# Performance work log

Measured on AMD Instinct MI355X. Metric: run time of the kernel, lower is better.

## Reference

```python
import jax, jax.numpy as jnp
import numpy as np

B, S, E = 4, 2048, 1024
N, H = 16, 64  # n_head, per-head hidden


def setup_inputs() -> dict:
    key = jax.random.key(0)
    k1, k2, k3, k4, k5 = jax.random.split(key, 5)
    scale_in = 1.0 / np.sqrt(E)
    scale_h = 1.0 / np.sqrt(N * H)
    return {
        "x": jax.random.normal(k1, (B, S, E), dtype=jnp.float32),
        "W_qkv": jax.random.uniform(k2, (E, 3 * N * H), minval=-scale_in, maxval=scale_in, dtype=jnp.float32),
        "b_qkv": jax.random.uniform(k3, (3 * N * H,), minval=-scale_in, maxval=scale_in, dtype=jnp.float32),
        "W_out": jax.random.uniform(k4, (N * H, E), minval=-scale_h, maxval=scale_h, dtype=jnp.float32),
        "b_out": jax.random.uniform(k5, (E,), minval=-scale_h, maxval=scale_h, dtype=jnp.float32),
    }


def reference(x, W_qkv, b_qkv, W_out, b_out):
    b, s, e = x.shape
    qkv = x @ W_qkv + b_qkv                      # [B,S,3NH]
    q, k, v = jnp.split(qkv, 3, axis=-1)
    q = q.reshape(b, s, N, H).transpose(0, 2, 1, 3)  # [B,N,S,H]
    k = k.reshape(b, s, N, H).transpose(0, 2, 1, 3)
    v = v.reshape(b, s, N, H).transpose(0, 2, 1, 3)
    inv_scale = jnp.asarray(1.0 / np.sqrt(H), dtype=x.dtype)
    attn = jnp.einsum('bnqh,bnkh->bnqk', q, k) * inv_scale  # [B,N,S,S]
    causal = jnp.tril(jnp.ones((s, s), dtype=bool))
    attn = jnp.where(causal[None, None], attn, jnp.asarray(-jnp.inf, dtype=attn.dtype))
    attn = jax.nn.softmax(attn, axis=-1)
    out = jnp.einsum('bnqk,bnkh->bnqh', attn, v)  # [B,N,S,H]
    out = out.transpose(0, 2, 1, 3).reshape(b, s, N * H)
    return out @ W_out + b_out
```

## Files before the change

kernel.cpp:

```cpp
#include <hip/hip_runtime.h>
#include <hip/hip_bf16.h>

typedef __attribute__((ext_vector_type(8))) short s16x8;
typedef __attribute__((ext_vector_type(4))) short s16x4;
typedef __attribute__((ext_vector_type(4))) float f32x4;

#define MFMA16(a, b, c) __builtin_amdgcn_mfma_f32_16x16x32_bf16(a, b, c, 0, 0, 0)

__device__ __forceinline__ short f2bf(float f) {
  unsigned int x = __builtin_bit_cast(unsigned int, f);
  x += 0x7fffu + ((x >> 16) & 1u);
  return (short)(x >> 16);
}

__device__ __forceinline__ int cperm(int k) {
  return ((k & 12) << 1) | ((k >> 4) << 2) | (k & 3);
}

#define LDT 40

__global__ void cvt_f32_bf16(const float* __restrict__ in, short* __restrict__ out, int n) {
  int idx = blockIdx.x * blockDim.x + threadIdx.x;
  int stride = gridDim.x * blockDim.x;
  for (int i = idx * 4; i < n; i += stride * 4) {
    float4 v = *(const float4*)(in + i);
    s16x4 o;
    o[0] = f2bf(v.x); o[1] = f2bf(v.y); o[2] = f2bf(v.z); o[3] = f2bf(v.w);
    *(s16x4*)(out + i) = o;
  }
}

__global__ __launch_bounds__(256) void gemm_qkv(
    const short* __restrict__ X, const short* __restrict__ W,
    const float* __restrict__ bias,
    short* __restrict__ Qo, short* __restrict__ Ko, short* __restrict__ Vo) {
  const int N = 3072, Kd = 1024;
  __shared__ short As[128 * LDT];
  __shared__ short Bs[128 * LDT];
  int t = threadIdx.x;
  int nTN = N / 128;
  int m0 = (blockIdx.x / nTN) * 128;
  int n0 = (blockIdx.x % nTN) * 128;
  int lane = t & 63, w = t >> 6;
  int wr = (w >> 1) * 64, wc = (w & 1) * 64;
  int r = lane & 15, g = lane >> 4;

  int ar = t >> 1;
  int ak = (t & 1) << 4;
  int bk = t & 31;
  int bc = (t >> 5) << 4;
  int cbk = cperm(bk);

  f32x4 acc[4][4];
  const f32x4 z4 = {0.f, 0.f, 0.f, 0.f};
#pragma unroll
  for (int i = 0; i < 4; ++i)
#pragma unroll
    for (int j = 0; j < 4; ++j) acc[i][j] = z4;

  for (int kt = 0; kt < Kd; kt += 32) {
    if (kt) __syncthreads();
    const short* xr = X + (size_t)(m0 + ar) * Kd + kt + ak;
    s16x8 va0 = *(const s16x8*)(xr);
    s16x8 va1 = *(const s16x8*)(xr + 8);
    short* Ad = &As[ar * LDT];
    *(s16x4*)(Ad + cperm(ak))      = __builtin_shufflevector(va0, va0, 0, 1, 2, 3);
    *(s16x4*)(Ad + cperm(ak + 4))  = __builtin_shufflevector(va0, va0, 4, 5, 6, 7);
    *(s16x4*)(Ad + cperm(ak + 8))  = __builtin_shufflevector(va1, va1, 0, 1, 2, 3);
    *(s16x4*)(Ad + cperm(ak + 12)) = __builtin_shufflevector(va1, va1, 4, 5, 6, 7);
    const short* wrp = W + (size_t)(kt + bk) * N + n0 + bc;
    s16x8 vb0 = *(const s16x8*)(wrp);
    s16x8 vb1 = *(const s16x8*)(wrp + 8);
#pragma unroll
    for (int i = 0; i < 8; ++i) Bs[(bc + i) * LDT + cbk] = vb0[i];
#pragma unroll
    for (int i = 0; i < 8; ++i) Bs[(bc + 8 + i) * LDT + cbk] = vb1[i];
    __syncthreads();

    s16x8 af[4], bfr[4];
#pragma unroll
    for (int mi = 0; mi < 4; ++mi)
      af[mi] = *(const s16x8*)(&As[(wr + mi * 16 + r) * LDT + g * 8]);
#pragma unroll
    for (int ni = 0; ni < 4; ++ni)
      bfr[ni] = *(const s16x8*)(&Bs[(wc + ni * 16 + r) * LDT + g * 8]);
#pragma unroll
    for (int mi = 0; mi < 4; ++mi)
#pragma unroll
      for (int ni = 0; ni < 4; ++ni)
        acc[mi][ni] = MFMA16(af[mi], bfr[ni], acc[mi][ni]);
  }

#pragma unroll
  for (int ni = 0; ni < 4; ++ni) {
    int col = n0 + wc + ni * 16 + r;
    float bv = bias[col];
    int which = col >> 10;
    int rem = col & 1023;
    int head = rem >> 6, h = rem & 63;
    short* dst = (which == 0) ? Qo : (which == 1) ? Ko : Vo;
#pragma unroll
    for (int mi = 0; mi < 4; ++mi)
#pragma unroll
      for (int e = 0; e < 4; ++e) {
        int row = m0 + wr + mi * 16 + g * 4 + e;
        int b = row >> 11, s = row & 2047;
        dst[((size_t)(b * 16 + head) * 2048 + s) * 64 + h] = f2bf(acc[mi][ni][e] + bv);
      }
  }
}

__global__ __launch_bounds__(256) void gemm_out(
    const short* __restrict__ X, const short* __restrict__ W,
    const float* __restrict__ bias, float* __restrict__ Out) {
  const int N = 1024, Kd = 1024;
  __shared__ short As[128 * LDT];
  __shared__ short Bs[128 * LDT];
  int t = threadIdx.x;
  int nTN = N / 128;
  int m0 = (blockIdx.x / nTN) * 128;
  int n0 = (blockIdx.x % nTN) * 128;
  int lane = t & 63, w = t >> 6;
  int wr = (w >> 1) * 64, wc = (w & 1) * 64;
  int r = lane & 15, g = lane >> 4;
  int ar = t >> 1, ak = (t & 1) << 4;
  int bk = t & 31, bc = (t >> 5) << 4;
  int cbk = cperm(bk);

  f32x4 acc[4][4];
  const f32x4 z4 = {0.f, 0.f, 0.f, 0.f};
#pragma unroll
  for (int i = 0; i < 4; ++i)
#pragma unroll
    for (int j = 0; j < 4; ++j) acc[i][j] = z4;

  for (int kt = 0; kt < Kd; kt += 32) {
    if (kt) __syncthreads();
    const short* xr = X + (size_t)(m0 + ar) * Kd + kt + ak;
    s16x8 va0 = *(const s16x8*)(xr);
    s16x8 va1 = *(const s16x8*)(xr + 8);
    short* Ad = &As[ar * LDT];
    *(s16x4*)(Ad + cperm(ak))      = __builtin_shufflevector(va0, va0, 0, 1, 2, 3);
    *(s16x4*)(Ad + cperm(ak + 4))  = __builtin_shufflevector(va0, va0, 4, 5, 6, 7);
    *(s16x4*)(Ad + cperm(ak + 8))  = __builtin_shufflevector(va1, va1, 0, 1, 2, 3);
    *(s16x4*)(Ad + cperm(ak + 12)) = __builtin_shufflevector(va1, va1, 4, 5, 6, 7);
    const short* wrp = W + (size_t)(kt + bk) * N + n0 + bc;
    s16x8 vb0 = *(const s16x8*)(wrp);
    s16x8 vb1 = *(const s16x8*)(wrp + 8);
#pragma unroll
    for (int i = 0; i < 8; ++i) Bs[(bc + i) * LDT + cbk] = vb0[i];
#pragma unroll
    for (int i = 0; i < 8; ++i) Bs[(bc + 8 + i) * LDT + cbk] = vb1[i];
    __syncthreads();

    s16x8 af[4], bfr[4];
#pragma unroll
    for (int mi = 0; mi < 4; ++mi)
      af[mi] = *(const s16x8*)(&As[(wr + mi * 16 + r) * LDT + g * 8]);
#pragma unroll
    for (int ni = 0; ni < 4; ++ni)
      bfr[ni] = *(const s16x8*)(&Bs[(wc + ni * 16 + r) * LDT + g * 8]);
#pragma unroll
    for (int mi = 0; mi < 4; ++mi)
#pragma unroll
      for (int ni = 0; ni < 4; ++ni)
        acc[mi][ni] = MFMA16(af[mi], bfr[ni], acc[mi][ni]);
  }

#pragma unroll
  for (int ni = 0; ni < 4; ++ni) {
    int col = n0 + wc + ni * 16 + r;
    float bv = bias[col];
#pragma unroll
    for (int mi = 0; mi < 4; ++mi)
#pragma unroll
      for (int e = 0; e < 4; ++e) {
        int row = m0 + wr + mi * 16 + g * 4 + e;
        Out[(size_t)row * N + col] = acc[mi][ni][e] + bv;
      }
  }
}

#define LDTV 72
__global__ __launch_bounds__(256) void attn(
    const short* __restrict__ Qb, const short* __restrict__ Kb,
    const short* __restrict__ Vb, short* __restrict__ Ob) {
  const int S = 2048, H = 64;
  int bid = blockIdx.x;
  int qt = 15 - (bid >> 6);
  int bn = bid & 63;
  int batch = bn >> 4, head = bn & 15;
  int q0 = qt * 128;
  int t = threadIdx.x, lane = t & 63, w = t >> 6;
  int r = lane & 15, g = lane >> 4;
  int qw = q0 + w * 32;

  const short* Qh = Qb + (size_t)bn * S * H;
  const short* Kh = Kb + (size_t)bn * S * H;
  const short* Vh = Vb + (size_t)bn * S * H;

  __shared__ short Vs[64 * LDTV];

  s16x8 qf[2][2];
#pragma unroll
  for (int n = 0; n < 2; ++n)
#pragma unroll
    for (int ks = 0; ks < 2; ++ks) {
      const short* qr = Qh + (size_t)(qw + n * 16 + r) * H + ks * 32 + g * 4;
      s16x4 lo = *(const s16x4*)(qr);
      s16x4 hi = *(const s16x4*)(qr + 16);
      qf[n][ks] = __builtin_shufflevector(lo, hi, 0, 1, 2, 3, 4, 5, 6, 7);
    }

  f32x4 o[2][4];
  const f32x4 z4 = {0.f, 0.f, 0.f, 0.f};
#pragma unroll
  for (int n = 0; n < 2; ++n)
#pragma unroll
    for (int hb = 0; hb < 4; ++hb) o[n][hb] = z4;
  float mrun[2] = {-__builtin_inff(), -__builtin_inff()};
  float lrun[2] = {0.f, 0.f};

  int ntiles = q0 / 64 + 2;

  int vr = lane;
  int hbase = w * 16;
  int vcol = ((vr >> 5) << 5) + cperm(vr & 31);

  s16x8 v0 = *(const s16x8*)(Vh + (size_t)vr * H + hbase);
  s16x8 v1 = *(const s16x8*)(Vh + (size_t)vr * H + hbase + 8);

  for (int tt = 0; tt < ntiles; ++tt) {
    int kv0 = tt * 64;
    if (tt) __syncthreads();
#pragma unroll
    for (int i = 0; i < 8; ++i) Vs[(hbase + i) * LDTV + vcol] = v0[i];
#pragma unroll
    for (int i = 0; i < 8; ++i) Vs[(hbase + 8 + i) * LDTV + vcol] = v1[i];
    __syncthreads();
    if (tt + 1 < ntiles) {
      const short* vp = Vh + (size_t)((tt + 1) * 64 + vr) * H + hbase;
      v0 = *(const s16x8*)(vp);
      v1 = *(const s16x8*)(vp + 8);
    }
    if (kv0 > qw + 31) continue;

    int mpmax = (qw + 31 - kv0) >> 4; if (mpmax > 3) mpmax = 3;
    bool need_mask = (kv0 + 63 > qw);

    s16x8 kf[4][2];
#pragma unroll
    for (int mp = 0; mp < 4; ++mp) {
      if (mp <= mpmax) {
#pragma unroll
        for (int ks = 0; ks < 2; ++ks) {
          const short* kr = Kh + (size_t)(kv0 + mp * 16 + r) * H + ks * 32 + g * 4;
          s16x4 lo = *(const s16x4*)(kr);
          s16x4 hi = *(const s16x4*)(kr + 16);
          kf[mp][ks] = __builtin_shufflevector(lo, hi, 0, 1, 2, 3, 4, 5, 6, 7);
        }
      }
    }

    float p[4][2][4];
    float rmax[2] = {-__builtin_inff(), -__builtin_inff()};
#pragma unroll
    for (int mp = 0; mp < 4; ++mp) {
      if (mp <= mpmax) {
        f32x4 st[2] = {z4, z4};
#pragma unroll
        for (int n = 0; n < 2; ++n)
#pragma unroll
          for (int ks = 0; ks < 2; ++ks)
            st[n] = MFMA16(kf[mp][ks], qf[n][ks], st[n]);
#pragma unroll
        for (int n = 0; n < 2; ++n)
#pragma unroll
          for (int e = 0; e < 4; ++e) {
            float v = st[n][e] * 0.125f;
            if (need_mask) {
              int kv = kv0 + mp * 16 + g * 4 + e;
              int q = qw + n * 16 + r;
              if (kv > q) v = -__builtin_inff();
            }
            p[mp][n][e] = v;
            rmax[n] = fmaxf(rmax[n], v);
          }
      } else {
#pragma unroll
        for (int n = 0; n < 2; ++n)
#pragma unroll
          for (int e = 0; e < 4; ++e) p[mp][n][e] = 0.f;
      }
    }

#pragma unroll
    for (int n = 0; n < 2; ++n) {
      rmax[n] = fmaxf(rmax[n], __shfl_xor(rmax[n], 16));
      rmax[n] = fmaxf(rmax[n], __shfl_xor(rmax[n], 32));
    }

#pragma unroll
    for (int n = 0; n < 2; ++n) {
      if (!__all(rmax[n] - mrun[n] <= 8.0f)) {
        float mnew = fmaxf(mrun[n], rmax[n]);
        float sc = __expf(mrun[n] - mnew);
        lrun[n] *= sc;
        mrun[n] = mnew;
#pragma unroll
        for (int e = 0; e < 4; ++e) {
          float bs = __shfl(sc, (lane & 48) + g * 4 + e);
#pragma unroll
          for (int hb = 0; hb < 4; ++hb) o[n][hb][e] *= bs;
        }
      }
    }

    float rsum[2] = {0.f, 0.f};
#pragma unroll
    for (int mp = 0; mp < 4; ++mp) {
      if (mp <= mpmax) {
#pragma unroll
        for (int n = 0; n < 2; ++n)
#pragma unroll
          for (int e = 0; e < 4; ++e) {
            float ev = __expf(p[mp][n][e] - mrun[n]);
            p[mp][n][e] = ev;
            rsum[n] += ev;
          }
      }
    }
#pragma unroll
    for (int n = 0; n < 2; ++n) {
      rsum[n] += __shfl_xor(rsum[n], 16);
      rsum[n] += __shfl_xor(rsum[n], 32);
      lrun[n] += rsum[n];
    }

    int kvhmax = mpmax >> 1;
#pragma unroll
    for (int kvh = 0; kvh < 2; ++kvh) {
      if (kvh > kvhmax) break;
      s16x8 pa[2];
#pragma unroll
      for (int n = 0; n < 2; ++n) {
        s16x8 tmp = {f2bf(p[2 * kvh][n][0]),     f2bf(p[2 * kvh][n][1]),
                     f2bf(p[2 * kvh][n][2]),     f2bf(p[2 * kvh][n][3]),
                     f2bf(p[2 * kvh + 1][n][0]), f2bf(p[2 * kvh + 1][n][1]),
                     f2bf(p[2 * kvh + 1][n][2]), f2bf(p[2 * kvh + 1][n][3])};
        pa[n] = tmp;
      }
#pragma unroll
      for (int hb = 0; hb < 4; ++hb) {
        s16x8 vf = *(const s16x8*)(&Vs[(hb * 16 + r) * LDTV + kvh * 32 + g * 8]);
#pragma unroll
        for (int n = 0; n < 2; ++n) o[n][hb] = MFMA16(pa[n], vf, o[n][hb]);
      }
    }
  }

#pragma unroll
  for (int n = 0; n < 2; ++n) {
    float il = 1.0f / lrun[n];
#pragma unroll
    for (int e = 0; e < 4; ++e) {
      float bv = __shfl(il, (lane & 48) + g * 4 + e);
      int s = qw + n * 16 + g * 4 + e;
#pragma unroll
      for (int hb = 0; hb < 4; ++hb) {
        int c = head * 64 + hb * 16 + r;
        Ob[(size_t)(batch * 2048 + s) * 1024 + c] = f2bf(o[n][hb][e] * bv);
      }
    }
  }
}

extern "C" void kernel_launch(void* const* d_in, const int* in_sizes, int n_in,
                              void* d_out, int out_size, void* d_ws, size_t ws_size,
                              hipStream_t stream) {
  const float* x    = (const float*)d_in[0];
  const float* Wqkv = (const float*)d_in[1];
  const float* bqkv = (const float*)d_in[2];
  const float* Wout = (const float*)d_in[3];
  const float* bout = (const float*)d_in[4];
  float* out = (float*)d_out;

  char* ws = (char*)d_ws;
  short* Xb    = (short*)(ws);
  short* Wqkvb = (short*)(ws + ((size_t)16 << 20));
  short* Woutb = (short*)(ws + ((size_t)22 << 20));
  short* Qb    = (short*)(ws + ((size_t)24 << 20));
  short* Kb    = (short*)(ws + ((size_t)40 << 20));
  short* Vb    = (short*)(ws + ((size_t)56 << 20));

  cvt_f32_bf16<<<2048, 256, 0, stream>>>(x, Xb, 4 * 2048 * 1024);
  cvt_f32_bf16<<<1024, 256, 0, stream>>>(Wqkv, 1024 * 3072 ? (short*)Wqkvb : Wqkvb, 1024 * 3072);
  cvt_f32_bf16<<<512, 256, 0, stream>>>(Wout, Woutb, 1024 * 1024);

  gemm_qkv<<<64 * 24, 256, 0, stream>>>(Xb, Wqkvb, bqkv, Qb, Kb, Vb);
  attn<<<64 * 16, 256, 0, stream>>>(Qb, Kb, Vb, Xb);
  gemm_out<<<64 * 8, 256, 0, stream>>>(Xb, Woutb, bout, out);
}
```

Before: 281.4 us.

## Pair causal query tiles per block, prefetch K fragments, fold scale into Q

Each attention block now handles two query tiles (qt and 15-qt), so every block does the same amount of causal work, and the grid is halved to 512 blocks. K fragments for the next tile are double-buffered in registers so their loads overlap the current tile's compute. The 1/sqrt(H) scale moves into the QKV GEMM epilogue, and the per-tile cross-lane row-sum reduction is deferred to the end. The cost is more register pressure from the two K buffers and fewer blocks in flight, which could lower occupancy.

```diff
diff --git a/kernel.cpp b/kernel.cpp
--- a/kernel.cpp
+++ b/kernel.cpp
@@ -99,13 +99,14 @@
     int rem = col & 1023;
     int head = rem >> 6, h = rem & 63;
     short* dst = (which == 0) ? Qo : (which == 1) ? Ko : Vo;
+    float qsc = (which == 0) ? 0.125f : 1.0f;
 #pragma unroll
     for (int mi = 0; mi < 4; ++mi)
 #pragma unroll
       for (int e = 0; e < 4; ++e) {
         int row = m0 + wr + mi * 16 + g * 4 + e;
         int b = row >> 11, s = row & 2047;
-        dst[((size_t)(b * 16 + head) * 2048 + s) * 64 + h] = f2bf(acc[mi][ni][e] + bv);
+        dst[((size_t)(b * 16 + head) * 2048 + s) * 64 + h] = f2bf((acc[mi][ni][e] + bv) * qsc);
       }
   }
 }
@@ -187,13 +188,11 @@
     const short* __restrict__ Vb, short* __restrict__ Ob) {
   const int S = 2048, H = 64;
   int bid = blockIdx.x;
-  int qt = 15 - (bid >> 6);
   int bn = bid & 63;
+  int pr = bid >> 6;
   int batch = bn >> 4, head = bn & 15;
-  int q0 = qt * 128;
   int t = threadIdx.x, lane = t & 63, w = t >> 6;
   int r = lane & 15, g = lane >> 4;
-  int qw = q0 + w * 32;
 
   const short* Qh = Qb + (size_t)bn * S * H;
   const short* Kh = Kb + (size_t)bn * S * H;
@@ -201,57 +200,40 @@
 
   __shared__ short Vs[64 * LDTV];
 
-  s16x8 qf[2][2];
-#pragma unroll
-  for (int n = 0; n < 2; ++n)
-#pragma unroll
-    for (int ks = 0; ks < 2; ++ks) {
-      const short* qr = Qh + (size_t)(qw + n * 16 + r) * H + ks * 32 + g * 4;
-      s16x4 lo = *(const s16x4*)(qr);
-      s16x4 hi = *(const s16x4*)(qr + 16);
-      qf[n][ks] = __builtin_shufflevector(lo, hi, 0, 1, 2, 3, 4, 5, 6, 7);
-    }
-
-  f32x4 o[2][4];
-  const f32x4 z4 = {0.f, 0.f, 0.f, 0.f};
-#pragma unroll
-  for (int n = 0; n < 2; ++n)
-#pragma unroll
-    for (int hb = 0; hb < 4; ++hb) o[n][hb] = z4;
-  float mrun[2] = {-__builtin_inff(), -__builtin_inff()};
-  float lrun[2] = {0.f, 0.f};
-
-  int ntiles = q0 / 64 + 2;
-
   int vr = lane;
   int hbase = w * 16;
   int vcol = ((vr >> 5) << 5) + cperm(vr & 31);
-
-  s16x8 v0 = *(const s16x8*)(Vh + (size_t)vr * H + hbase);
-  s16x8 v1 = *(const s16x8*)(Vh + (size_t)vr * H + hbase + 8);
-
-  for (int tt = 0; tt < ntiles; ++tt) {
-    int kv0 = tt * 64;
-    if (tt) __syncthreads();
-#pragma unroll
-    for (int i = 0; i < 8; ++i) Vs[(hbase + i) * LDTV + vcol] = v0[i];
-#pragma unroll
-    for (int i = 0; i < 8; ++i) Vs[(hbase + 8 + i) * LDTV + vcol] = v1[i];
-    __syncthreads();
-    if (tt + 1 < ntiles) {
-      const short* vp = Vh + (size_t)((tt + 1) * 64 + vr) * H + hbase;
-      v0 = *(const s16x8*)(vp);
-      v1 = *(const s16x8*)(vp + 8);
-    }
-    if (kv0 > qw + 31) continue;
-
-    int mpmax = (qw + 31 - kv0) >> 4; if (mpmax > 3) mpmax = 3;
-    bool need_mask = (kv0 + 63 > qw);
-
-    s16x8 kf[4][2];
-#pragma unroll
-    for (int mp = 0; mp < 4; ++mp) {
-      if (mp <= mpmax) {
+  const f32x4 z4 = {0.f, 0.f, 0.f, 0.f};
+
+#pragma unroll
+  for (int ph = 0; ph < 2; ++ph) {
+    int qt = ph ? pr : (15 - pr);
+    int q0 = qt * 128;
+    int qw = q0 + w * 32;
+    int ntiles = qt * 2 + 2;
+
+    s16x8 qf[2][2];
+#pragma unroll
+    for (int n = 0; n < 2; ++n)
+#pragma unroll
+      for (int ks = 0; ks < 2; ++ks) {
+        const short* qr = Qh + (size_t)(qw + n * 16 + r) * H + ks * 32 + g * 4;
+        s16x4 lo = *(const s16x4*)(qr);
+        s16x4 hi = *(const s16x4*)(qr + 16);
+        qf[n][ks] = __builtin_shufflevector(lo, hi, 0, 1, 2, 3, 4, 5, 6, 7);
+      }
+
+    f32x4 o[2][4];
+#pragma unroll
+    for (int n = 0; n < 2; ++n)
+#pragma unroll
+      for (int hb = 0; hb < 4; ++hb) o[n][hb] = z4;
+    float mrun[2] = {-__builtin_inff(), -__builtin_inff()};
+    float lsum[2] = {0.f, 0.f};
+
+    auto LOADK = [&](int kv0, s16x8 (&kf)[4][2]) {
+#pragma unroll
+      for (int mp = 0; mp < 4; ++mp)
 #pragma unroll
         for (int ks = 0; ks < 2; ++ks) {
           const short* kr = Kh + (size_t)(kv0 + mp * 16 + r) * H + ks * 32 + g * 4;
@@ -259,117 +241,143 @@
           s16x4 hi = *(const s16x4*)(kr + 16);
           kf[mp][ks] = __builtin_shufflevector(lo, hi, 0, 1, 2, 3, 4, 5, 6, 7);
         }
-      }
+    };
+
+    s16x8 v0 = *(const s16x8*)(Vh + (size_t)vr * H + hbase);
+    s16x8 v1 = *(const s16x8*)(Vh + (size_t)vr * H + hbase + 8);
+    s16x8 kfA[4][2], kfB[4][2];
+    LOADK(0, kfA);
+
+    auto TILE = [&](int tt, s16x8 (&kfc)[4][2], s16x8 (&kfn)[4][2]) {
+      int kv0 = tt * 64;
+      if (tt | ph) __syncthreads();
+#pragma unroll
+      for (int i = 0; i < 8; ++i) Vs[(hbase + i) * LDTV + vcol] = v0[i];
+#pragma unroll
+      for (int i = 0; i < 8; ++i) Vs[(hbase + 8 + i) * LDTV + vcol] = v1[i];
+      __syncthreads();
+      if (tt + 1 < ntiles) {
+        const short* vp = Vh + (size_t)((tt + 1) * 64 + vr) * H + hbase;
+        v0 = *(const s16x8*)(vp);
+        v1 = *(const s16x8*)(vp + 8);
+      }
+      int tn = tt + 1;
+      if (tn < ntiles && tn * 64 <= qw + 31) LOADK(tn * 64, kfn);
+      if (kv0 > qw + 31) return;
+
+      int mpmax = (qw + 31 - kv0) >> 4; if (mpmax > 3) mpmax = 3;
+      bool need_mask = (kv0 + 63 > qw);
+
+      float p[4][2][4];
+      float rmax[2] = {-__builtin_inff(), -__builtin_inff()};
+#pragma unroll
+      for (int mp = 0; mp < 4; ++mp) {
+        if (mp <= mpmax) {
+          f32x4 st[2] = {z4, z4};
+#pragma unroll
+          for (int n = 0; n < 2; ++n)
+#pragma unroll
+            for (int ks = 0; ks < 2; ++ks)
+              st[n] = MFMA16(kfc[mp][ks], qf[n][ks], st[n]);
+#pragma unroll
+          for (int n = 0; n < 2; ++n)
+#pragma unroll
+            for (int e = 0; e < 4; ++e) {
+              float v = st[n][e];
+              if (need_mask) {
+                int kv = kv0 + mp * 16 + g * 4 + e;
+                int q = qw + n * 16 + r;
+                if (kv > q) v = -__builtin_inff();
+              }
+              p[mp][n][e] = v;
+              rmax[n] = fmaxf(rmax[n], v);
+            }
+        } else {
+#pragma unroll
+          for (int n = 0; n < 2; ++n)
+#pragma unroll
+            for (int e = 0; e < 4; ++e) p[mp][n][e] = 0.f;
+        }
+      }
+
+#pragma unroll
+      for (int n = 0; n < 2; ++n) {
+        rmax[n] = fmaxf(rmax[n], __shfl_xor(rmax[n], 16));
+        rmax[n] = fmaxf(rmax[n], __shfl_xor(rmax[n], 32));
+      }
+
+#pragma unroll
+      for (int n = 0; n < 2; ++n) {
+        if (!__all(rmax[n] - mrun[n] <= 8.0f)) {
+          float mnew = fmaxf(mrun[n], rmax[n]);
+          float sc = __expf(mrun[n] - mnew);
+          lsum[n] *= sc;
+          mrun[n] = mnew;
+#pragma unroll
+          for (int e = 0; e < 4; ++e) {
+            float bs = __shfl(sc, (lane & 48) + g * 4 + e);
+#pragma unroll
+            for (int hb = 0; hb < 4; ++hb) o[n][hb][e] *= bs;
+          }
+        }
+      }
+
+#pragma unroll
+      for (int mp = 0; mp < 4; ++mp) {
+        if (mp <= mpmax) {
+#pragma unroll
+          for (int n = 0; n < 2; ++n)
+#pragma unroll
+            for (int e = 0; e < 4; ++e) {
+              float ev = __expf(p[mp][n][e] - mrun[n]);
+              p[mp][n][e] = ev;
+              lsum[n] += ev;
+            }
+        }
+      }
+
+      int kvhmax = mpmax >> 1;
+#pragma unroll
+      for (int kvh = 0; kvh < 2; ++kvh) {
+        if (kvh > kvhmax) break;
+        s16x8 pa[2];
+#pragma unroll
+        for (int n = 0; n < 2; ++n) {
+          s16x8 tmp = {f2bf(p[2 * kvh][n][0]),     f2bf(p[2 * kvh][n][1]),
+                       f2bf(p[2 * kvh][n][2]),     f2bf(p[2 * kvh][n][3]),
+                       f2bf(p[2 * kvh + 1][n][0]), f2bf(p[2 * kvh + 1][n][1]),
+                       f2bf(p[2 * kvh + 1][n][2]), f2bf(p[2 * kvh + 1][n][3])};
+          pa[n] = tmp;
+        }
+#pragma unroll
+        for (int hb = 0; hb < 4; ++hb) {
+          s16x8 vf = *(const s16x8*)(&Vs[(hb * 16 + r) * LDTV + kvh * 32 + g * 8]);
+#pragma unroll
+          for (int n = 0; n < 2; ++n) o[n][hb] = MFMA16(pa[n], vf, o[n][hb]);
+        }
+      }
+    };
+
+    for (int tt = 0; tt < ntiles; tt += 2) {
+      TILE(tt, kfA, kfB);
+      TILE(tt + 1, kfB, kfA);
     }
 
-    float p[4][2][4];
-    float rmax[2] = {-__builtin_inff(), -__builtin_inff()};
-#pragma unroll
-    for (int mp = 0; mp < 4; ++mp) {
-      if (mp <= mpmax) {
-        f32x4 st[2] = {z4, z4};
-#pragma unroll
-        for (int n = 0; n < 2; ++n)
-#pragma unroll
-          for (int ks = 0; ks < 2; ++ks)
-            st[n] = MFMA16(kf[mp][ks], qf[n][ks], st[n]);
-#pragma unroll
-        for (int n = 0; n < 2; ++n)
-#pragma unroll
-          for (int e = 0; e < 4; ++e) {
-            float v = st[n][e] * 0.125f;
-            if (need_mask) {
-              int kv = kv0 + mp * 16 + g * 4 + e;
-              int q = qw + n * 16 + r;
-              if (kv > q) v = -__builtin_inff();
-            }
-            p[mp][n][e] = v;
-            rmax[n] = fmaxf(rmax[n], v);
-          }
-      } else {
-#pragma unroll
-        for (int n = 0; n < 2; ++n)
-#pragma unroll
-          for (int e = 0; e < 4; ++e) p[mp][n][e] = 0.f;
-      }
-    }
-
 #pragma unroll
     for (int n = 0; n < 2; ++n) {
-      rmax[n] = fmaxf(rmax[n], __shfl_xor(rmax[n], 16));
-      rmax[n] = fmaxf(rmax[n], __shfl_xor(rmax[n], 32));
-    }
-
-#pragma unroll
-    for (int n = 0; n < 2; ++n) {
-      if (!__all(rmax[n] - mrun[n] <= 8.0f)) {
-        float mnew = fmaxf(mrun[n], rmax[n]);
-        float sc = __expf(mrun[n] - mnew);
-        lrun[n] *= sc;
-        mrun[n] = mnew;
-#pragma unroll
-        for (int e = 0; e < 4; ++e) {
-          float bs = __shfl(sc, (lane & 48) + g * 4 + e);
-#pragma unroll
-          for (int hb = 0; hb < 4; ++hb) o[n][hb][e] *= bs;
-        }
-      }
-    }
-
-    float rsum[2] = {0.f, 0.f};
-#pragma unroll
-    for (int mp = 0; mp < 4; ++mp) {
-      if (mp <= mpmax) {
-#pragma unroll
-        for (int n = 0; n < 2; ++n)
-#pragma unroll
-          for (int e = 0; e < 4; ++e) {
-            float ev = __expf(p[mp][n][e] - mrun[n]);
-            p[mp][n][e] = ev;
-            rsum[n] += ev;
-          }
-      }
-    }
-#pragma unroll
-    for (int n = 0; n < 2; ++n) {
-      rsum[n] += __shfl_xor(rsum[n], 16);
-      rsum[n] += __shfl_xor(rsum[n], 32);
-      lrun[n] += rsum[n];
-    }
-
-    int kvhmax = mpmax >> 1;
-#pragma unroll
-    for (int kvh = 0; kvh < 2; ++kvh) {
-      if (kvh > kvhmax) break;
-      s16x8 pa[2];
-#pragma unroll
-      for (int n = 0; n < 2; ++n) {
-        s16x8 tmp = {f2bf(p[2 * kvh][n][0]),     f2bf(p[2 * kvh][n][1]),
-                     f2bf(p[2 * kvh][n][2]),     f2bf(p[2 * kvh][n][3]),
-                     f2bf(p[2 * kvh + 1][n][0]), f2bf(p[2 * kvh + 1][n][1]),
-                     f2bf(p[2 * kvh + 1][n][2]), f2bf(p[2 * kvh + 1][n][3])};
-        pa[n] = tmp;
-      }
-#pragma unroll
-      for (int hb = 0; hb < 4; ++hb) {
-        s16x8 vf = *(const s16x8*)(&Vs[(hb * 16 + r) * LDTV + kvh * 32 + g * 8]);
-#pragma unroll
-        for (int n = 0; n < 2; ++n) o[n][hb] = MFMA16(pa[n], vf, o[n][hb]);
-      }
-    }
-  }
-
-#pragma unroll
-  for (int n = 0; n < 2; ++n) {
-    float il = 1.0f / lrun[n];
-#pragma unroll
-    for (int e = 0; e < 4; ++e) {
-      float bv = __shfl(il, (lane & 48) + g * 4 + e);
-      int s = qw + n * 16 + g * 4 + e;
-#pragma unroll
-      for (int hb = 0; hb < 4; ++hb) {
-        int c = head * 64 + hb * 16 + r;
-        Ob[(size_t)(batch * 2048 + s) * 1024 + c] = f2bf(o[n][hb][e] * bv);
+      float lt = lsum[n];
+      lt += __shfl_xor(lt, 16);
+      lt += __shfl_xor(lt, 32);
+      float il = 1.0f / lt;
+#pragma unroll
+      for (int e = 0; e < 4; ++e) {
+        float bv = __shfl(il, (lane & 48) + g * 4 + e);
+        int s = qw + n * 16 + g * 4 + e;
+#pragma unroll
+        for (int hb = 0; hb < 4; ++hb) {
+          int c = head * 64 + hb * 16 + r;
+          Ob[(size_t)(batch * 2048 + s) * 1024 + c] = f2bf(o[n][hb][e] * bv);
+        }
       }
     }
   }
@@ -394,10 +402,10 @@
   short* Vb    = (short*)(ws + ((size_t)56 << 20));
 
   cvt_f32_bf16<<<2048, 256, 0, stream>>>(x, Xb, 4 * 2048 * 1024);
-  cvt_f32_bf16<<<1024, 256, 0, stream>>>(Wqkv, 1024 * 3072 ? (short*)Wqkvb : Wqkvb, 1024 * 3072);
+  cvt_f32_bf16<<<1024, 256, 0, stream>>>(Wqkv, Wqkvb, 1024 * 3072);
   cvt_f32_bf16<<<512, 256, 0, stream>>>(Wout, Woutb, 1024 * 1024);
 
   gemm_qkv<<<64 * 24, 256, 0, stream>>>(Xb, Wqkvb, bqkv, Qb, Kb, Vb);
-  attn<<<64 * 16, 256, 0, stream>>>(Qb, Kb, Vb, Xb);
+  attn<<<512, 256, 0, stream>>>(Qb, Kb, Vb, Xb);
   gemm_out<<<64 * 8, 256, 0, stream>>>(Xb, Woutb, bout, out);
 }
```

Measured after the change: 283.5 us. About the same (+0.7%).
